# Kernel tuning notes

Hardware: AMD Instinct MI355X
Metric: run time of the kernel (lower is better)

The kernel has to match this reference:

```python
import jax, jax.numpy as jnp
import numpy as np
import math

B, MSA, L, D = 1, 64, 256, 512
H = 8
DH = D // H  # 64


def setup_inputs() -> dict:
    key = jax.random.key(0)
    ks = jax.random.split(key, 6)
    x = jax.random.normal(ks[0], (B, MSA, L, D), dtype=jnp.float32)
    Wq = jax.random.normal(ks[1], (D, D), dtype=jnp.float32) * (1.0 / math.sqrt(D))
    Wk = jax.random.normal(ks[2], (D, D), dtype=jnp.float32) * (1.0 / math.sqrt(D))
    Wv = jax.random.normal(ks[3], (D, D), dtype=jnp.float32) * (1.0 / math.sqrt(D))
    aK = jax.random.normal(ks[4], (L, L, DH), dtype=jnp.float32)
    aV = jax.random.normal(ks[5], (L, L, DH), dtype=jnp.float32)
    return {"x": x, "Wq": Wq, "Wk": Wk, "Wv": Wv, "aK": aK, "aV": aV}


def _proj(t, W, b, m, l, h, dh):
    # nn.Linear(bias=False): t @ W.T, then split heads -> (B,H,MSA,L,dh)
    y = jnp.einsum('bmld,ed->bmle', t, W).reshape(b, m, l, h, dh)
    return jnp.transpose(y, (0, 3, 1, 2, 4))


def reference(x, Wq, Wk, Wv, aK, aV):
    b, m, l, d = x.shape
    h, dh = H, DH
    q = _proj(x, Wq, b, m, l, h, dh)  # (B,H,MSA,L,dh)
    k = _proj(x, Wk, b, m, l, h, dh)
    v = _proj(x, Wv, b, m, l, h, dh)
    # content score + relative-position score
    e1 = jnp.einsum('bhmid,bhmjd->bhmij', q, k)           # (B,H,MSA,L,L)
    e2 = jnp.einsum('bhmid,ijd->bhmij', q, aK)            # (B,H,MSA,L,L)
    alpha = jax.nn.softmax((e1 + e2) / math.sqrt(dh), axis=-1)
    z1 = jnp.einsum('bhmij,bhmjd->bhmid', alpha, v)       # content output
    z2 = jnp.einsum('bhmij,ijd->bhmid', alpha, aV)        # relative-V output
    z = (z1 + z2).sum(axis=2)                             # sum over MSA -> (B,H,L,dh)
    out = jnp.transpose(z, (0, 2, 1, 3)).reshape(b, l, d) # (B,L,D)
    return out
```

## Files before the change

kernel.cpp:

```cpp
#include <hip/hip_runtime.h>

#define THREADS 256

typedef unsigned short u16;
typedef __attribute__((ext_vector_type(8))) short bf16x8;
typedef __attribute__((ext_vector_type(4))) float f32x4;

__device__ __forceinline__ u16 f2bf(float f) {
  unsigned int u = __float_as_uint(f);
  u += 0x7fffu + ((u >> 16) & 1u);
  return (u16)(u >> 16);
}
__device__ __forceinline__ float bf2f(u16 s) {
  return __uint_as_float(((unsigned int)s) << 16);
}
__device__ __forceinline__ bf16x8 ld8g(const u16* p) {
  return *reinterpret_cast<const bf16x8*>(p);
}
__device__ __forceinline__ bf16x8 ld8s(const u16* p) {
  return *reinterpret_cast<const bf16x8*>(p);
}
__device__ __forceinline__ void st4bf(u16* dst, float4 v) {
  unsigned int lo = (unsigned int)f2bf(v.x) | ((unsigned int)f2bf(v.y) << 16);
  unsigned int hi = (unsigned int)f2bf(v.z) | ((unsigned int)f2bf(v.w) << 16);
  uint2 u; u.x = lo; u.y = hi;
  *reinterpret_cast<uint2*>(dst) = u;
}
__device__ __forceinline__ uint4 pack8(float4 a, float4 b) {
  uint4 r;
  r.x = (unsigned int)f2bf(a.x) | ((unsigned int)f2bf(a.y) << 16);
  r.y = (unsigned int)f2bf(a.z) | ((unsigned int)f2bf(a.w) << 16);
  r.z = (unsigned int)f2bf(b.x) | ((unsigned int)f2bf(b.y) << 16);
  r.w = (unsigned int)f2bf(b.z) | ((unsigned int)f2bf(b.w) << 16);
  return r;
}
typedef __attribute__((address_space(1))) const unsigned int g_u32;
typedef __attribute__((address_space(3))) unsigned int l_u32;
__device__ __forceinline__ void async16(const u16* g, u16* l) {
  __builtin_amdgcn_global_load_lds((g_u32*)g, (l_u32*)l, 16, 0, 0);
}


__global__ __launch_bounds__(THREADS) void cast_xw(
    const float* __restrict__ x, const float* __restrict__ wq,
    const float* __restrict__ wk, const float* __restrict__ wv,
    u16* __restrict__ xb, u16* __restrict__ wqb, u16* __restrict__ wkb,
    u16* __restrict__ wvb) {
  int t = blockIdx.x * THREADS + threadIdx.x;
  if (t < 2097152) {
    st4bf(xb + t * 4, reinterpret_cast<const float4*>(x)[t]);
  } else if (t < 2162688) {
    int q = t - 2097152;
    st4bf(wqb + q * 4, reinterpret_cast<const float4*>(wq)[q]);
  } else if (t < 2228224) {
    int q = t - 2162688;
    st4bf(wkb + q * 4, reinterpret_cast<const float4*>(wk)[q]);
  } else if (t < 2293760) {
    int q = t - 2228224;
    st4bf(wvb + q * 4, reinterpret_cast<const float4*>(wv)[q]);
  }
}

__global__ __launch_bounds__(THREADS) void proj_gemm(
    const u16* __restrict__ xb, const u16* __restrict__ wb,
    u16* __restrict__ qh, u16* __restrict__ kb, u16* __restrict__ vt) {
  const int bm = blockIdx.x / 12, bn = blockIdx.x % 12;
  const int tid = threadIdx.x;
  const int wave = tid >> 6, lane = tid & 63;
  const int quad = lane >> 4, l15 = lane & 15;
  __shared__ __align__(16) u16 smem[9216];
  u16* At = smem;
  u16* Bt = smem + 4096;

  const int rowL = lane >> 2;
  const int chunkL = (lane & 3) ^ ((lane >> 3) & 3);
  const u16* gA = xb + (size_t)(bm * 128 + wave * 32 + rowL) * 512 + chunkL * 8;
  const u16* gB = wb + (size_t)(bn * 128 + wave * 32 + rowL) * 512 + chunkL * 8;
  u16* lA = At + wave * 1024;
  u16* lB = Bt + wave * 1024;

  const int rw0 = (wave & 1) * 64, cw0 = (wave >> 1) * 64;
  const int swz = (quad ^ ((l15 >> 1) & 3)) * 8;

  f32x4 acc[4][4];
#pragma unroll
  for (int mt = 0; mt < 4; ++mt)
#pragma unroll
    for (int nt = 0; nt < 4; ++nt) acc[mt][nt] = (f32x4){0.f, 0.f, 0.f, 0.f};

  for (int s = 0; s < 16; ++s) {
    __syncthreads();
    async16(gA + s * 32, lA);
    async16(gA + s * 32 + 8192, lA + 512);
    async16(gB + s * 32, lB);
    async16(gB + s * 32 + 8192, lB + 512);
    __syncthreads();
    bf16x8 af[4], bf[4];
#pragma unroll
    for (int mt = 0; mt < 4; ++mt)
      af[mt] = ld8s(At + (rw0 + mt * 16 + l15) * 32 + swz);
#pragma unroll
    for (int nt = 0; nt < 4; ++nt)
      bf[nt] = ld8s(Bt + (cw0 + nt * 16 + l15) * 32 + swz);
#pragma unroll
    for (int mt = 0; mt < 4; ++mt)
#pragma unroll
      for (int nt = 0; nt < 4; ++nt)
        acc[mt][nt] = __builtin_amdgcn_mfma_f32_16x16x32_bf16(af[mt], bf[nt], acc[mt][nt], 0, 0, 0);
  }

  const int mat = bn >> 2;
  const int h0 = (bn & 3) * 2;
  const int m = bm >> 1;
  const int l0 = (bm & 1) * 128;

  if (mat < 2) {
    u16* dstb = (mat == 0) ? qh : kb;
    const int il = tid >> 1, cc = (tid & 1) * 32;
#pragma unroll
    for (int p = 0; p < 2; ++p) {
      __syncthreads();
      if ((wave >> 1) == p) {
#pragma unroll
        for (int mt = 0; mt < 4; ++mt)
#pragma unroll
          for (int nt = 0; nt < 4; ++nt)
#pragma unroll
            for (int r = 0; r < 4; ++r)
              smem[(rw0 + mt * 16 + quad * 4 + r) * 72 + nt * 16 + l15] =
                  f2bf(acc[mt][nt][r]);
      }
      __syncthreads();
      u16* dst = dstb + ((size_t)((h0 + p) * 64 + m) * 256 + l0 + il) * 64 + cc;
      uint4 v0 = *reinterpret_cast<uint4*>(&smem[il * 72 + cc]);
      uint4 v1 = *reinterpret_cast<uint4*>(&smem[il * 72 + cc + 8]);
      uint4 v2 = *reinterpret_cast<uint4*>(&smem[il * 72 + cc + 16]);
      uint4 v3 = *reinterpret_cast<uint4*>(&smem[il * 72 + cc + 24]);
      *reinterpret_cast<uint4*>(dst) = v0;
      *reinterpret_cast<uint4*>(dst + 8) = v1;
      *reinterpret_cast<uint4*>(dst + 16) = v2;
      *reinterpret_cast<uint4*>(dst + 24) = v3;
    }
  } else {
    const int tl = tid >> 2, cc = (tid & 3) * 32;
#pragma unroll
    for (int p = 0; p < 2; ++p) {
      __syncthreads();
      if ((wave >> 1) == p) {
#pragma unroll
        for (int mt = 0; mt < 4; ++mt)
#pragma unroll
          for (int nt = 0; nt < 4; ++nt)
#pragma unroll
            for (int r = 0; r < 4; ++r)
              smem[(nt * 16 + l15) * 136 + rw0 + mt * 16 + quad * 4 + r] =
                  f2bf(acc[mt][nt][r]);
      }
      __syncthreads();
      int hm = (h0 + p) * 64 + m;
      u16* dst = vt + (size_t)hm * 16384 + tl * 256 + l0 + cc;
      uint4 v0 = *reinterpret_cast<uint4*>(&smem[tl * 136 + cc]);
      uint4 v1 = *reinterpret_cast<uint4*>(&smem[tl * 136 + cc + 8]);
      uint4 v2 = *reinterpret_cast<uint4*>(&smem[tl * 136 + cc + 16]);
      uint4 v3 = *reinterpret_cast<uint4*>(&smem[tl * 136 + cc + 24]);
      *reinterpret_cast<uint4*>(dst) = v0;
      *reinterpret_cast<uint4*>(dst + 8) = v1;
      *reinterpret_cast<uint4*>(dst + 16) = v2;
      *reinterpret_cast<uint4*>(dst + 24) = v3;
    }
  }
}

__global__ __launch_bounds__(THREADS) void e2_k(
    const u16* __restrict__ qh, const float* __restrict__ aK,
    u16* __restrict__ e2c) {
  const int i = blockIdx.x >> 3, hmt = blockIdx.x & 7;
  const int tid = threadIdx.x;
  const int wave = tid >> 6, lane = tid & 63;
  const int quad = lane >> 4, l15 = lane & 15;
  __shared__ u16 aKl[256 * 72];
#pragma unroll
  for (int c = 0; c < 8; ++c) {
    int fidx = c * 2048 + tid * 8;
    int j = fidx >> 6, d = fidx & 63;
    float4 f0 = *reinterpret_cast<const float4*>(aK + (size_t)i * 16384 + fidx);
    float4 f1 = *reinterpret_cast<const float4*>(aK + (size_t)i * 16384 + fidx + 4);
    *reinterpret_cast<uint4*>(&aKl[j * 72 + d]) = pack8(f0, f1);
  }
  __syncthreads();
  f32x4 acc[16];
#pragma unroll
  for (int nt = 0; nt < 16; ++nt) acc[nt] = (f32x4){0.f, 0.f, 0.f, 0.f};
  bf16x8 a[2];
#pragma unroll
  for (int ks = 0; ks < 2; ++ks)
    a[ks] = ld8g(qh + ((size_t)(hmt * 64 + wave * 16 + l15) * 256 + i) * 64 + ks * 32 + quad * 8);
#pragma unroll
  for (int nt = 0; nt < 16; ++nt) {
#pragma unroll
    for (int ks = 0; ks < 2; ++ks) {
      bf16x8 b = ld8s(&aKl[(nt * 16 + l15) * 72 + ks * 32 + quad * 8]);
      acc[nt] = __builtin_amdgcn_mfma_f32_16x16x32_bf16(a[ks], b, acc[nt], 0, 0, 0);
    }
  }
  const int it = i >> 6, wt = (i >> 4) & 3, qt = (i >> 2) & 3, rt = i & 3;
  u16* ebase = e2c + (size_t)(qt * 16 + l15) * 64 + rt * 16;
#pragma unroll
  for (int re = 0; re < 4; ++re) {
    int hm = hmt * 64 + wave * 16 + quad * 4 + re;
    u16 buf[16];
#pragma unroll
    for (int nt = 0; nt < 16; ++nt) buf[nt] = f2bf(acc[nt][re]);
    u16* d = ebase + ((size_t)(hm * 4 + it) * 4 + wt) * 4096;
    reinterpret_cast<uint4*>(d)[0] = reinterpret_cast<uint4*>(buf)[0];
    reinterpret_cast<uint4*>(d)[1] = reinterpret_cast<uint4*>(buf)[1];
  }
}

__global__ __launch_bounds__(THREADS) void attn_k(
    const u16* __restrict__ qh, const u16* __restrict__ kb,
    const u16* __restrict__ vt, u16* __restrict__ e2c,
    u16* __restrict__ z1p) {
  const int bi = blockIdx.x;
  const int hm = bi & 511, it = bi >> 9;
  const int tid = threadIdx.x;
  const int wave = tid >> 6, lane = tid & 63;
  const int quad = lane >> 4, l15 = lane & 15;
  __shared__ u16 As[4 * 4224];
  u16* W = &As[wave * 4224];

  u16* eb = e2c + (((size_t)hm * 4 + it) * 4 + wave) * 4096 + (size_t)lane * 64;
  uint4 e2v[8];
#pragma unroll
  for (int c = 0; c < 8; ++c) e2v[c] = reinterpret_cast<const uint4*>(eb)[c];
  const u16* e2a = reinterpret_cast<const u16*>(e2v);

  f32x4 acc[16];
#pragma unroll
  for (int nt = 0; nt < 16; ++nt) acc[nt] = (f32x4){0.f, 0.f, 0.f, 0.f};
  bf16x8 a[2];
#pragma unroll
  for (int ks = 0; ks < 2; ++ks)
    a[ks] = ld8g(qh + ((size_t)hm * 256 + it * 64 + wave * 16 + l15) * 64 + ks * 32 + quad * 8);
#pragma unroll
  for (int nt = 0; nt < 16; ++nt) {
#pragma unroll
    for (int ks = 0; ks < 2; ++ks) {
      bf16x8 b = ld8g(kb + ((size_t)hm * 256 + nt * 16 + l15) * 64 + ks * 32 + quad * 8);
      acc[nt] = __builtin_amdgcn_mfma_f32_16x16x32_bf16(a[ks], b, acc[nt], 0, 0, 0);
    }
  }
#pragma unroll
  for (int nt = 0; nt < 16; ++nt)
#pragma unroll
    for (int r = 0; r < 4; ++r)
      acc[nt][r] = (acc[nt][r] + bf2f(e2a[r * 16 + nt])) * 0.125f;

  u16 a16[64];
#pragma unroll
  for (int r = 0; r < 4; ++r) {
    float mx = -3.0e38f;
#pragma unroll
    for (int nt = 0; nt < 16; ++nt) mx = fmaxf(mx, acc[nt][r]);
    for (int msk = 1; msk < 16; msk <<= 1) mx = fmaxf(mx, __shfl_xor(mx, msk));
    float s = 0.f;
#pragma unroll
    for (int nt = 0; nt < 16; ++nt) {
      float p = __expf(acc[nt][r] - mx);
      acc[nt][r] = p;
      s += p;
    }
    for (int msk = 1; msk < 16; msk <<= 1) s += __shfl_xor(s, msk);
    float inv = 1.0f / s;
    int lrow = quad * 4 + r;
#pragma unroll
    for (int nt = 0; nt < 16; ++nt) {
      u16 pb = f2bf(acc[nt][r] * inv);
      a16[r * 16 + nt] = pb;
      W[lrow * 264 + nt * 16 + l15] = pb;
    }
  }
#pragma unroll
  for (int c = 0; c < 8; ++c)
    reinterpret_cast<uint4*>(eb)[c] = reinterpret_cast<const uint4*>(a16)[c];

  f32x4 acc2[4];
#pragma unroll
  for (int nt = 0; nt < 4; ++nt) acc2[nt] = (f32x4){0.f, 0.f, 0.f, 0.f};
#pragma unroll
  for (int ks = 0; ks < 8; ++ks) {
    bf16x8 a2 = ld8s(&W[l15 * 264 + ks * 32 + quad * 8]);
#pragma unroll
    for (int nt = 0; nt < 4; ++nt) {
      bf16x8 b2 = ld8g(vt + (size_t)hm * 16384 + (nt * 16 + l15) * 256 + ks * 32 + quad * 8);
      acc2[nt] = __builtin_amdgcn_mfma_f32_16x16x32_bf16(a2, b2, acc2[nt], 0, 0, 0);
    }
  }
#pragma unroll
  for (int nt = 0; nt < 4; ++nt)
#pragma unroll
    for (int r = 0; r < 4; ++r)
      W[(quad * 4 + r) * 264 + nt * 16 + l15] = f2bf(acc2[nt][r]);
  {
    int row = lane >> 2, col = (lane & 3) * 16;
    uint4 v0 = *reinterpret_cast<uint4*>(&W[row * 264 + col]);
    uint4 v1 = *reinterpret_cast<uint4*>(&W[row * 264 + col + 8]);
    u16* dst = z1p + (size_t)hm * 16384 + (it * 64 + wave * 16 + row) * 64 + col;
    *reinterpret_cast<uint4*>(dst) = v0;
    *reinterpret_cast<uint4*>(dst + 8) = v1;
  }
}

__global__ __launch_bounds__(THREADS) void beta_k(
    const u16* __restrict__ alphac, float* __restrict__ beta) {
  const int b = blockIdx.x;
  const int h = b >> 6, it = (b >> 4) & 3, wt = (b >> 2) & 3, qt = b & 3;
  const int tid = threadIdx.x;
  const int l15 = tid >> 4, sub = tid & 15, r = sub >> 2, ntq = sub & 3;
  const u16* base = alphac + ((size_t)((h * 64) * 4 + it) * 4 + wt) * 4096 +
                    (size_t)(qt * 16 + l15) * 64 + r * 16 + ntq * 4;
  float s0 = 0.f, s1 = 0.f, s2 = 0.f, s3 = 0.f;
#pragma unroll 8
  for (int m = 0; m < 64; ++m) {
    uint2 v = *reinterpret_cast<const uint2*>(base + (size_t)m * 65536);
    const u16* p = reinterpret_cast<const u16*>(&v);
    s0 += bf2f(p[0]); s1 += bf2f(p[1]); s2 += bf2f(p[2]); s3 += bf2f(p[3]);
  }
  const int i = it * 64 + wt * 16 + qt * 4 + r;
  float* o = beta + ((size_t)h * 256 + i) * 256 + l15;
  o[(ntq * 4 + 0) * 16] = s0;
  o[(ntq * 4 + 1) * 16] = s1;
  o[(ntq * 4 + 2) * 16] = s2;
  o[(ntq * 4 + 3) * 16] = s3;
}

__global__ __launch_bounds__(THREADS) void z2_k(
    const float* __restrict__ beta, const float* __restrict__ aV,
    float* __restrict__ z2b) {
  const int i = blockIdx.x;
  const int tid = threadIdx.x;
  const int wave = tid >> 6, lane = tid & 63;
  const int quad = lane >> 4, l15 = lane & 15;
  __shared__ u16 aVl[64 * 264];
#pragma unroll
  for (int c = 0; c < 8; ++c) {
    int fidx = c * 2048 + tid * 8;
    int j = fidx >> 6, d = fidx & 63;
    float4 f0 = *reinterpret_cast<const float4*>(aV + (size_t)i * 16384 + fidx);
    float4 f1 = *reinterpret_cast<const float4*>(aV + (size_t)i * 16384 + fidx + 4);
    float fv[8] = {f0.x, f0.y, f0.z, f0.w, f1.x, f1.y, f1.z, f1.w};
#pragma unroll
    for (int u = 0; u < 8; ++u) aVl[(d + u) * 264 + j] = f2bf(fv[u]);
  }
  __syncthreads();
  f32x4 acc = (f32x4){0.f, 0.f, 0.f, 0.f};
#pragma unroll
  for (int ks = 0; ks < 8; ++ks) {
    u16 ab[8];
    if (l15 < 8) {
      const float* bp = beta + ((size_t)l15 * 256 + i) * 256 + ks * 32 + quad * 8;
      float4 f0 = *reinterpret_cast<const float4*>(bp);
      float4 f1 = *reinterpret_cast<const float4*>(bp + 4);
      ab[0] = f2bf(f0.x); ab[1] = f2bf(f0.y); ab[2] = f2bf(f0.z); ab[3] = f2bf(f0.w);
      ab[4] = f2bf(f1.x); ab[5] = f2bf(f1.y); ab[6] = f2bf(f1.z); ab[7] = f2bf(f1.w);
    } else {
#pragma unroll
      for (int u = 0; u < 8; ++u) ab[u] = 0;
    }
    bf16x8 a = *reinterpret_cast<bf16x8*>(ab);
    bf16x8 b = ld8s(&aVl[(wave * 16 + l15) * 264 + ks * 32 + quad * 8]);
    acc = __builtin_amdgcn_mfma_f32_16x16x32_bf16(a, b, acc, 0, 0, 0);
  }
#pragma unroll
  for (int r = 0; r < 4; ++r) {
    int h = quad * 4 + r;
    if (h < 8) z2b[(size_t)i * 512 + h * 64 + wave * 16 + l15] = acc[r];
  }
}

__global__ __launch_bounds__(THREADS) void reduce_k(
    const u16* __restrict__ z1p, const float* __restrict__ z2b,
    float* __restrict__ out) {
  int t = blockIdx.x * THREADS + threadIdx.x;
  size_t o8 = (size_t)t * 8;
  int i = (int)(o8 >> 9), e0 = (int)(o8 & 511);
  int h = e0 >> 6, d0 = e0 & 63;
  float4 s0 = reinterpret_cast<const float4*>(z2b + o8)[0];
  float4 s1 = reinterpret_cast<const float4*>(z2b + o8)[1];
  float s[8] = {s0.x, s0.y, s0.z, s0.w, s1.x, s1.y, s1.z, s1.w};
  const u16* zb = z1p + (size_t)h * 64 * 16384 + (size_t)i * 64 + d0;
#pragma unroll 4
  for (int m = 0; m < 64; ++m) {
    uint4 v = *reinterpret_cast<const uint4*>(zb + (size_t)m * 16384);
    const u16* p = reinterpret_cast<const u16*>(&v);
#pragma unroll
    for (int k = 0; k < 8; ++k) s[k] += bf2f(p[k]);
  }
  float4 r0 = {s[0], s[1], s[2], s[3]}, r1 = {s[4], s[5], s[6], s[7]};
  reinterpret_cast<float4*>(out + o8)[0] = r0;
  reinterpret_cast<float4*>(out + o8)[1] = r1;
}

extern "C" void kernel_launch(void* const* d_in, const int* in_sizes, int n_in,
                              void* d_out, int out_size, void* d_ws, size_t ws_size,
                              hipStream_t stream) {
  const float* x  = (const float*)d_in[0];
  const float* wq = (const float*)d_in[1];
  const float* wk = (const float*)d_in[2];
  const float* wv = (const float*)d_in[3];
  const float* aK = (const float*)d_in[4];
  const float* aV = (const float*)d_in[5];
  float* out = (float*)d_out;

  char* ws = (char*)d_ws;
  u16* xb    = (u16*)(ws + 0);
  u16* wqb   = (u16*)(ws + 16777216);
  u16* wkb   = (u16*)(ws + 17301504);
  u16* wvb   = (u16*)(ws + 17825792);
  float* beta= (float*)(ws + 18350080);
  float* z2b = (float*)(ws + 20447232);
  u16* qh    = (u16*)(ws + 35127296);
  u16* kb    = (u16*)(ws + 51904512);
  u16* vt    = (u16*)(ws + 68681728);
  u16* e2c   = (u16*)(ws + 85458944);
  u16* z1p   = xb;

  cast_xw<<<8960, THREADS, 0, stream>>>(x, wq, wk, wv, xb, wqb, wkb, wvb);
  proj_gemm<<<1536, THREADS, 0, stream>>>(xb, wqb, qh, kb, vt);
  e2_k<<<2048, THREADS, 0, stream>>>(qh, aK, e2c);
  attn_k<<<2048, THREADS, 0, stream>>>(qh, kb, vt, e2c, z1p);
  beta_k<<<512, THREADS, 0, stream>>>(e2c, beta);
  z2_k<<<256, THREADS, 0, stream>>>(beta, aV, z2b);
  reduce_k<<<64, THREADS, 0, stream>>>(z1p, z2b, out);
}
```

Baseline: 309.6 us.

## Fuse beta, z2 and final reduction into one tail kernel; prefetch first V tile

The three tail kernels (MSA-sum of alpha into beta, the beta×aV product, and the MSA-sum of z1 plus z2) are merged into one kernel with 256 blocks, one per query row. Beta and z2 now stay in shared memory instead of round-tripping through global workspace, which also removes two launches. In the attention kernel, the first k-slice of V is loaded before the softmax so its latency overlaps that work. The cost is more shared memory per block and lower parallelism in the final reduction: 256 blocks doing 2-element loads instead of 64 blocks doing 16-byte loads.

```diff
diff --git a/kernel.cpp b/kernel.cpp
--- a/kernel.cpp
+++ b/kernel.cpp
@@ -256,6 +256,11 @@
     for (int r = 0; r < 4; ++r)
       acc[nt][r] = (acc[nt][r] + bf2f(e2a[r * 16 + nt])) * 0.125f;
 
+  bf16x8 b2p[4];
+#pragma unroll
+  for (int nt = 0; nt < 4; ++nt)
+    b2p[nt] = ld8g(vt + (size_t)hm * 16384 + (nt * 16 + l15) * 256 + quad * 8);
+
   u16 a16[64];
 #pragma unroll
   for (int r = 0; r < 4; ++r) {
@@ -292,7 +297,8 @@
     bf16x8 a2 = ld8s(&W[l15 * 264 + ks * 32 + quad * 8]);
 #pragma unroll
     for (int nt = 0; nt < 4; ++nt) {
-      bf16x8 b2 = ld8g(vt + (size_t)hm * 16384 + (nt * 16 + l15) * 256 + ks * 32 + quad * 8);
+      bf16x8 b2 = (ks == 0) ? b2p[nt]
+          : ld8g(vt + (size_t)hm * 16384 + (nt * 16 + l15) * 256 + ks * 32 + quad * 8);
       acc2[nt] = __builtin_amdgcn_mfma_f32_16x16x32_bf16(a2, b2, acc2[nt], 0, 0, 0);
     }
   }
@@ -311,37 +317,17 @@
   }
 }
 
-__global__ __launch_bounds__(THREADS) void beta_k(
-    const u16* __restrict__ alphac, float* __restrict__ beta) {
-  const int b = blockIdx.x;
-  const int h = b >> 6, it = (b >> 4) & 3, wt = (b >> 2) & 3, qt = b & 3;
-  const int tid = threadIdx.x;
-  const int l15 = tid >> 4, sub = tid & 15, r = sub >> 2, ntq = sub & 3;
-  const u16* base = alphac + ((size_t)((h * 64) * 4 + it) * 4 + wt) * 4096 +
-                    (size_t)(qt * 16 + l15) * 64 + r * 16 + ntq * 4;
-  float s0 = 0.f, s1 = 0.f, s2 = 0.f, s3 = 0.f;
-#pragma unroll 8
-  for (int m = 0; m < 64; ++m) {
-    uint2 v = *reinterpret_cast<const uint2*>(base + (size_t)m * 65536);
-    const u16* p = reinterpret_cast<const u16*>(&v);
-    s0 += bf2f(p[0]); s1 += bf2f(p[1]); s2 += bf2f(p[2]); s3 += bf2f(p[3]);
-  }
-  const int i = it * 64 + wt * 16 + qt * 4 + r;
-  float* o = beta + ((size_t)h * 256 + i) * 256 + l15;
-  o[(ntq * 4 + 0) * 16] = s0;
-  o[(ntq * 4 + 1) * 16] = s1;
-  o[(ntq * 4 + 2) * 16] = s2;
-  o[(ntq * 4 + 3) * 16] = s3;
-}
-
-__global__ __launch_bounds__(THREADS) void z2_k(
-    const float* __restrict__ beta, const float* __restrict__ aV,
-    float* __restrict__ z2b) {
+__global__ __launch_bounds__(THREADS) void tail_k(
+    const u16* __restrict__ alphac, const float* __restrict__ aV,
+    const u16* __restrict__ z1p, float* __restrict__ out) {
   const int i = blockIdx.x;
+  const int it = i >> 6, wt = (i >> 4) & 3, qt = (i >> 2) & 3, r = i & 3;
   const int tid = threadIdx.x;
   const int wave = tid >> 6, lane = tid & 63;
   const int quad = lane >> 4, l15 = lane & 15;
   __shared__ u16 aVl[64 * 264];
+  __shared__ float betaL[8 * 264];
+  __shared__ float z2L[512];
 #pragma unroll
   for (int c = 0; c < 8; ++c) {
     int fidx = c * 2048 + tid * 8;
@@ -352,53 +338,60 @@
 #pragma unroll
     for (int u = 0; u < 8; ++u) aVl[(d + u) * 264 + j] = f2bf(fv[u]);
   }
+  {
+    const int h = tid >> 5, u = tid & 31, l15b = u >> 1, nh = u & 1;
+    const u16* base = alphac + (((size_t)(h * 64) * 4 + it) * 4 + wt) * 4096 +
+                      (size_t)(qt * 16 + l15b) * 64 + r * 16 + nh * 8;
+    float s[8] = {0.f, 0.f, 0.f, 0.f, 0.f, 0.f, 0.f, 0.f};
+    for (int m = 0; m < 64; ++m) {
+      uint4 v = *reinterpret_cast<const uint4*>(base + (size_t)m * 65536);
+      const u16* p = reinterpret_cast<const u16*>(&v);
+#pragma unroll
+      for (int k = 0; k < 8; ++k) s[k] += bf2f(p[k]);
+    }
+#pragma unroll
+    for (int k = 0; k < 8; ++k)
+      betaL[h * 264 + (nh * 8 + k) * 16 + l15b] = s[k];
+  }
   __syncthreads();
-  f32x4 acc = (f32x4){0.f, 0.f, 0.f, 0.f};
-#pragma unroll
-  for (int ks = 0; ks < 8; ++ks) {
-    u16 ab[8];
-    if (l15 < 8) {
-      const float* bp = beta + ((size_t)l15 * 256 + i) * 256 + ks * 32 + quad * 8;
-      float4 f0 = *reinterpret_cast<const float4*>(bp);
-      float4 f1 = *reinterpret_cast<const float4*>(bp + 4);
-      ab[0] = f2bf(f0.x); ab[1] = f2bf(f0.y); ab[2] = f2bf(f0.z); ab[3] = f2bf(f0.w);
-      ab[4] = f2bf(f1.x); ab[5] = f2bf(f1.y); ab[6] = f2bf(f1.z); ab[7] = f2bf(f1.w);
-    } else {
-#pragma unroll
-      for (int u = 0; u < 8; ++u) ab[u] = 0;
-    }
-    bf16x8 a = *reinterpret_cast<bf16x8*>(ab);
-    bf16x8 b = ld8s(&aVl[(wave * 16 + l15) * 264 + ks * 32 + quad * 8]);
-    acc = __builtin_amdgcn_mfma_f32_16x16x32_bf16(a, b, acc, 0, 0, 0);
-  }
-#pragma unroll
-  for (int r = 0; r < 4; ++r) {
-    int h = quad * 4 + r;
-    if (h < 8) z2b[(size_t)i * 512 + h * 64 + wave * 16 + l15] = acc[r];
-  }
-}
-
-__global__ __launch_bounds__(THREADS) void reduce_k(
-    const u16* __restrict__ z1p, const float* __restrict__ z2b,
-    float* __restrict__ out) {
-  int t = blockIdx.x * THREADS + threadIdx.x;
-  size_t o8 = (size_t)t * 8;
-  int i = (int)(o8 >> 9), e0 = (int)(o8 & 511);
-  int h = e0 >> 6, d0 = e0 & 63;
-  float4 s0 = reinterpret_cast<const float4*>(z2b + o8)[0];
-  float4 s1 = reinterpret_cast<const float4*>(z2b + o8)[1];
-  float s[8] = {s0.x, s0.y, s0.z, s0.w, s1.x, s1.y, s1.z, s1.w};
-  const u16* zb = z1p + (size_t)h * 64 * 16384 + (size_t)i * 64 + d0;
-#pragma unroll 4
-  for (int m = 0; m < 64; ++m) {
-    uint4 v = *reinterpret_cast<const uint4*>(zb + (size_t)m * 16384);
-    const u16* p = reinterpret_cast<const u16*>(&v);
-#pragma unroll
-    for (int k = 0; k < 8; ++k) s[k] += bf2f(p[k]);
-  }
-  float4 r0 = {s[0], s[1], s[2], s[3]}, r1 = {s[4], s[5], s[6], s[7]};
-  reinterpret_cast<float4*>(out + o8)[0] = r0;
-  reinterpret_cast<float4*>(out + o8)[1] = r1;
+  {
+    f32x4 acc = (f32x4){0.f, 0.f, 0.f, 0.f};
+#pragma unroll
+    for (int ks = 0; ks < 8; ++ks) {
+      u16 ab[8];
+      if (l15 < 8) {
+        const float* bp = &betaL[l15 * 264 + ks * 32 + quad * 8];
+#pragma unroll
+        for (int u2 = 0; u2 < 8; ++u2) ab[u2] = f2bf(bp[u2]);
+      } else {
+#pragma unroll
+        for (int u2 = 0; u2 < 8; ++u2) ab[u2] = 0;
+      }
+      bf16x8 a = *reinterpret_cast<bf16x8*>(ab);
+      bf16x8 b = ld8s(&aVl[(wave * 16 + l15) * 264 + ks * 32 + quad * 8]);
+      acc = __builtin_amdgcn_mfma_f32_16x16x32_bf16(a, b, acc, 0, 0, 0);
+    }
+#pragma unroll
+    for (int rr = 0; rr < 4; ++rr) {
+      int h = quad * 4 + rr;
+      if (h < 8) z2L[h * 64 + wave * 16 + l15] = acc[rr];
+    }
+  }
+  __syncthreads();
+  {
+    int e0 = tid * 2;
+    int h = e0 >> 6, d0 = e0 & 63;
+    float s0 = z2L[e0], s1 = z2L[e0 + 1];
+    const u16* zb = z1p + (size_t)(h * 64) * 16384 + (size_t)i * 64 + d0;
+#pragma unroll 8
+    for (int m = 0; m < 64; ++m) {
+      unsigned int v = *reinterpret_cast<const unsigned int*>(zb + (size_t)m * 16384);
+      s0 += bf2f((u16)(v & 0xffff));
+      s1 += bf2f((u16)(v >> 16));
+    }
+    float2 o = {s0, s1};
+    *reinterpret_cast<float2*>(out + (size_t)i * 512 + e0) = o;
+  }
 }
 
 extern "C" void kernel_launch(void* const* d_in, const int* in_sizes, int n_in,
@@ -417,8 +410,6 @@
   u16* wqb   = (u16*)(ws + 16777216);
   u16* wkb   = (u16*)(ws + 17301504);
   u16* wvb   = (u16*)(ws + 17825792);
-  float* beta= (float*)(ws + 18350080);
-  float* z2b = (float*)(ws + 20447232);
   u16* qh    = (u16*)(ws + 35127296);
   u16* kb    = (u16*)(ws + 51904512);
   u16* vt    = (u16*)(ws + 68681728);
@@ -429,7 +420,5 @@
   proj_gemm<<<1536, THREADS, 0, stream>>>(xb, wqb, qh, kb, vt);
   e2_k<<<2048, THREADS, 0, stream>>>(qh, aK, e2c);
   attn_k<<<2048, THREADS, 0, stream>>>(qh, kb, vt, e2c, z1p);
-  beta_k<<<512, THREADS, 0, stream>>>(e2c, beta);
-  z2_k<<<256, THREADS, 0, stream>>>(beta, aV, z2b);
-  reduce_k<<<64, THREADS, 0, stream>>>(z1p, z2b, out);
-}
+  tail_k<<<256, THREADS, 0, stream>>>(e2c, aV, z1p, out);
+}
```

Result: slower. 329.4 us (+6.4%).

## Split MSA reductions across more blocks and prefetch first V tile in attention

Applied to the files above, without the earlier changes.

beta_k now splits the 64-row MSA sum into four partial chunks across four times as many blocks and writes partial betas in an i-major layout. z2_k sums the four partials while loading. reduce_k moves from 8 outputs per thread to one output per thread, which gives eight times more blocks at the cost of narrower 2-byte loads. In attn_k the first k-step of V fragments is loaded before the softmax to hide global load latency. The aim is to fill the GPU better in the small tail kernels, in exchange for extra partial-sum traffic and less vectorised loads.

```diff
diff --git a/kernel.cpp b/kernel.cpp
--- a/kernel.cpp
+++ b/kernel.cpp
@@ -256,6 +256,11 @@
     for (int r = 0; r < 4; ++r)
       acc[nt][r] = (acc[nt][r] + bf2f(e2a[r * 16 + nt])) * 0.125f;
 
+  bf16x8 b2p[4];
+#pragma unroll
+  for (int nt = 0; nt < 4; ++nt)
+    b2p[nt] = ld8g(vt + (size_t)hm * 16384 + (nt * 16 + l15) * 256 + quad * 8);
+
   u16 a16[64];
 #pragma unroll
   for (int r = 0; r < 4; ++r) {
@@ -292,7 +297,8 @@
     bf16x8 a2 = ld8s(&W[l15 * 264 + ks * 32 + quad * 8]);
 #pragma unroll
     for (int nt = 0; nt < 4; ++nt) {
-      bf16x8 b2 = ld8g(vt + (size_t)hm * 16384 + (nt * 16 + l15) * 256 + ks * 32 + quad * 8);
+      bf16x8 b2 = (ks == 0) ? b2p[nt]
+          : ld8g(vt + (size_t)hm * 16384 + (nt * 16 + l15) * 256 + ks * 32 + quad * 8);
       acc2[nt] = __builtin_amdgcn_mfma_f32_16x16x32_bf16(a2, b2, acc2[nt], 0, 0, 0);
     }
   }
@@ -312,22 +318,24 @@
 }
 
 __global__ __launch_bounds__(THREADS) void beta_k(
-    const u16* __restrict__ alphac, float* __restrict__ beta) {
+    const u16* __restrict__ alphac, float* __restrict__ betap) {
   const int b = blockIdx.x;
-  const int h = b >> 6, it = (b >> 4) & 3, wt = (b >> 2) & 3, qt = b & 3;
+  const int slice = b >> 2, mc = b & 3;
+  const int h = slice >> 6, it = (slice >> 4) & 3, wt = (slice >> 2) & 3, qt = slice & 3;
   const int tid = threadIdx.x;
-  const int l15 = tid >> 4, sub = tid & 15, r = sub >> 2, ntq = sub & 3;
-  const u16* base = alphac + ((size_t)((h * 64) * 4 + it) * 4 + wt) * 4096 +
-                    (size_t)(qt * 16 + l15) * 64 + r * 16 + ntq * 4;
+  const int l15b = tid >> 4, sub = tid & 15, r = sub >> 2, ntq = sub & 3;
+  const u16* base = alphac +
+      (((size_t)(h * 64 + mc * 16) * 4 + it) * 4 + wt) * 4096 +
+      (size_t)(qt * 16 + l15b) * 64 + r * 16 + ntq * 4;
   float s0 = 0.f, s1 = 0.f, s2 = 0.f, s3 = 0.f;
 #pragma unroll 8
-  for (int m = 0; m < 64; ++m) {
+  for (int m = 0; m < 16; ++m) {
     uint2 v = *reinterpret_cast<const uint2*>(base + (size_t)m * 65536);
     const u16* p = reinterpret_cast<const u16*>(&v);
     s0 += bf2f(p[0]); s1 += bf2f(p[1]); s2 += bf2f(p[2]); s3 += bf2f(p[3]);
   }
   const int i = it * 64 + wt * 16 + qt * 4 + r;
-  float* o = beta + ((size_t)h * 256 + i) * 256 + l15;
+  float* o = betap + (size_t)mc * 524288 + ((size_t)i * 8 + h) * 256 + l15b;
   o[(ntq * 4 + 0) * 16] = s0;
   o[(ntq * 4 + 1) * 16] = s1;
   o[(ntq * 4 + 2) * 16] = s2;
@@ -335,7 +343,7 @@
 }
 
 __global__ __launch_bounds__(THREADS) void z2_k(
-    const float* __restrict__ beta, const float* __restrict__ aV,
+    const float* __restrict__ betap, const float* __restrict__ aV,
     float* __restrict__ z2b) {
   const int i = blockIdx.x;
   const int tid = threadIdx.x;
@@ -358,14 +366,21 @@
   for (int ks = 0; ks < 8; ++ks) {
     u16 ab[8];
     if (l15 < 8) {
-      const float* bp = beta + ((size_t)l15 * 256 + i) * 256 + ks * 32 + quad * 8;
-      float4 f0 = *reinterpret_cast<const float4*>(bp);
-      float4 f1 = *reinterpret_cast<const float4*>(bp + 4);
-      ab[0] = f2bf(f0.x); ab[1] = f2bf(f0.y); ab[2] = f2bf(f0.z); ab[3] = f2bf(f0.w);
-      ab[4] = f2bf(f1.x); ab[5] = f2bf(f1.y); ab[6] = f2bf(f1.z); ab[7] = f2bf(f1.w);
+      float s[8] = {0.f, 0.f, 0.f, 0.f, 0.f, 0.f, 0.f, 0.f};
+#pragma unroll
+      for (int mc = 0; mc < 4; ++mc) {
+        const float* bp = betap + (size_t)mc * 524288 +
+                          ((size_t)i * 8 + l15) * 256 + ks * 32 + quad * 8;
+        float4 f0 = *reinterpret_cast<const float4*>(bp);
+        float4 f1 = *reinterpret_cast<const float4*>(bp + 4);
+        s[0] += f0.x; s[1] += f0.y; s[2] += f0.z; s[3] += f0.w;
+        s[4] += f1.x; s[5] += f1.y; s[6] += f1.z; s[7] += f1.w;
+      }
+#pragma unroll
+      for (int u2 = 0; u2 < 8; ++u2) ab[u2] = f2bf(s[u2]);
     } else {
 #pragma unroll
-      for (int u = 0; u < 8; ++u) ab[u] = 0;
+      for (int u2 = 0; u2 < 8; ++u2) ab[u2] = 0;
     }
     bf16x8 a = *reinterpret_cast<bf16x8*>(ab);
     bf16x8 b = ld8s(&aVl[(wave * 16 + l15) * 264 + ks * 32 + quad * 8]);
@@ -381,24 +396,14 @@
 __global__ __launch_bounds__(THREADS) void reduce_k(
     const u16* __restrict__ z1p, const float* __restrict__ z2b,
     float* __restrict__ out) {
-  int t = blockIdx.x * THREADS + threadIdx.x;
-  size_t o8 = (size_t)t * 8;
-  int i = (int)(o8 >> 9), e0 = (int)(o8 & 511);
-  int h = e0 >> 6, d0 = e0 & 63;
-  float4 s0 = reinterpret_cast<const float4*>(z2b + o8)[0];
-  float4 s1 = reinterpret_cast<const float4*>(z2b + o8)[1];
-  float s[8] = {s0.x, s0.y, s0.z, s0.w, s1.x, s1.y, s1.z, s1.w};
-  const u16* zb = z1p + (size_t)h * 64 * 16384 + (size_t)i * 64 + d0;
-#pragma unroll 4
-  for (int m = 0; m < 64; ++m) {
-    uint4 v = *reinterpret_cast<const uint4*>(zb + (size_t)m * 16384);
-    const u16* p = reinterpret_cast<const u16*>(&v);
-#pragma unroll
-    for (int k = 0; k < 8; ++k) s[k] += bf2f(p[k]);
-  }
-  float4 r0 = {s[0], s[1], s[2], s[3]}, r1 = {s[4], s[5], s[6], s[7]};
-  reinterpret_cast<float4*>(out + o8)[0] = r0;
-  reinterpret_cast<float4*>(out + o8)[1] = r1;
+  int o = blockIdx.x * THREADS + threadIdx.x;
+  int i = o >> 9, e = o & 511;
+  int h = e >> 6, d = e & 63;
+  float s = z2b[o];
+  const u16* base = z1p + (size_t)(h * 64) * 16384 + (size_t)i * 64 + d;
+#pragma unroll 8
+  for (int m = 0; m < 64; ++m) s += bf2f(base[(size_t)m * 16384]);
+  out[o] = s;
 }
 
 extern "C" void kernel_launch(void* const* d_in, const int* in_sizes, int n_in,
@@ -413,23 +418,23 @@
   float* out = (float*)d_out;
 
   char* ws = (char*)d_ws;
-  u16* xb    = (u16*)(ws + 0);
-  u16* wqb   = (u16*)(ws + 16777216);
-  u16* wkb   = (u16*)(ws + 17301504);
-  u16* wvb   = (u16*)(ws + 17825792);
-  float* beta= (float*)(ws + 18350080);
-  float* z2b = (float*)(ws + 20447232);
-  u16* qh    = (u16*)(ws + 35127296);
-  u16* kb    = (u16*)(ws + 51904512);
-  u16* vt    = (u16*)(ws + 68681728);
-  u16* e2c   = (u16*)(ws + 85458944);
-  u16* z1p   = xb;
+  u16* xb     = (u16*)(ws + 0);
+  u16* wqb    = (u16*)(ws + 16777216);
+  u16* wkb    = (u16*)(ws + 17301504);
+  u16* wvb    = (u16*)(ws + 17825792);
+  float* betap= (float*)(ws + 18350080);
+  float* z2b  = (float*)(ws + 26738688);
+  u16* qh     = (u16*)(ws + 35127296);
+  u16* kb     = (u16*)(ws + 51904512);
+  u16* vt     = (u16*)(ws + 68681728);
+  u16* e2c    = (u16*)(ws + 85458944);
+  u16* z1p    = xb;
 
   cast_xw<<<8960, THREADS, 0, stream>>>(x, wq, wk, wv, xb, wqb, wkb, wvb);
   proj_gemm<<<1536, THREADS, 0, stream>>>(xb, wqb, qh, kb, vt);
   e2_k<<<2048, THREADS, 0, stream>>>(qh, aK, e2c);
   attn_k<<<2048, THREADS, 0, stream>>>(qh, kb, vt, e2c, z1p);
-  beta_k<<<512, THREADS, 0, stream>>>(e2c, beta);
-  z2_k<<<256, THREADS, 0, stream>>>(beta, aV, z2b);
-  reduce_k<<<64, THREADS, 0, stream>>>(z1p, z2b, out);
-}
+  beta_k<<<2048, THREADS, 0, stream>>>(e2c, betap);
+  z2_k<<<256, THREADS, 0, stream>>>(betap, aV, z2b);
+  reduce_k<<<512, THREADS, 0, stream>>>(z1p, z2b, out);
+}
```

Result: no change. 308.5 us (-0.4%).
